# Kernel tuning notes

Hardware: AMD Instinct MI355X
Metric: run time of the kernel (lower is better)

The kernel has to match this reference:

```python
import jax, jax.numpy as jnp
import numpy as np

EPS = 1e-6
NEG_SLOPE = 0.2
LN_EPS = 1e-6


def _evn_nonlinearity(x, wa, ba, wb, bb):
    # x: (..., F, D); norm over the vector axis F (axis=-2)
    norm = jnp.linalg.norm(x, axis=-2, keepdims=True)  # (..., 1, D)
    zero_norm = norm <= EPS
    norm = norm + EPS
    h = jax.nn.leaky_relu(norm @ wa + ba, NEG_SLOPE)   # (..., 1, D//2)
    g = h @ wb + bb                                    # (..., 1, D)
    # skip_connection == 0: rescale direction by learned norm gate
    return jnp.where(zero_norm, x, x / norm * g)


def _layernorm(x, scale, bias):
    mean = jnp.mean(x, axis=-1, keepdims=True)
    var = jnp.var(x, axis=-1, keepdims=True)
    return (x - mean) * jax.lax.rsqrt(var + LN_EPS) * scale + bias


def setup_inputs() -> dict:
    key = jax.random.key(0)
    ks = jax.random.split(key, 12)
    B, N, F, D = 8, 2048, 3, 256
    QK, V, H, Q = 512, 512, 8, 64
    dh, dv = QK // H, V // H
    s = lambda *sh: 1.0 / np.sqrt(sh[0])
    return {
        "x": jax.random.normal(ks[0], (B, N, F, D), jnp.float32),
        "lq": jax.random.normal(ks[1], (Q, QK), jnp.float32) * s(QK),
        "w_kv": jax.random.normal(ks[2], (D, QK), jnp.float32) * s(D),
        "w_evn1a": jax.random.normal(ks[3], (QK, QK // 2), jnp.float32) * s(QK),
        "b_evn1a": jnp.zeros((QK // 2,), jnp.float32),
        "w_evn1b": jax.random.normal(ks[4], (QK // 2, QK), jnp.float32) * s(QK // 2),
        "b_evn1b": jnp.zeros((QK,), jnp.float32),
        "wq": jax.random.normal(ks[5], (QK, H, dh), jnp.float32) * s(QK),
        "wk": jax.random.normal(ks[6], (QK, H, dh), jnp.float32) * s(QK),
        "wv": jax.random.normal(ks[7], (QK, H, dv), jnp.float32) * s(QK),
        "ln_q_scale": jnp.ones((dh,), jnp.float32),
        "ln_q_bias": jnp.zeros((dh,), jnp.float32),
        "ln_k_scale": jnp.ones((dh,), jnp.float32),
        "ln_k_bias": jnp.zeros((dh,), jnp.float32),
        "w_out": jax.random.normal(ks[8], (V, V), jnp.float32) * s(V),
        "w_evn2a": jax.random.normal(ks[9], (V, V // 2), jnp.float32) * s(V),
        "b_evn2a": jnp.zeros((V // 2,), jnp.float32),
        "w_evn2b": jax.random.normal(ks[10], (V // 2, V), jnp.float32) * s(V // 2),
        "b_evn2b": jnp.zeros((V,), jnp.float32),
    }


def reference(x, lq, w_kv, w_evn1a, b_evn1a, w_evn1b, b_evn1b, wq, wk, wv,
              ln_q_scale, ln_q_bias, ln_k_scale, ln_k_bias,
              w_out, w_evn2a, b_evn2a, w_evn2b, b_evn2b):
    B, N, F, _ = x.shape
    H = wq.shape[1]
    # EVLinearLeakyReLU: Dense (no bias) + EVN nonlinearity
    kv = _evn_nonlinearity(x @ w_kv, w_evn1a, b_evn1a, w_evn1b, b_evn1b)  # (B,N,F,QK)
    # invariant features: contract vector axis with its channel-mean
    kv_inv = jnp.einsum('bnfd,bnf->bnd', kv, jnp.mean(kv, axis=-1))       # (B,N,QK)
    q = jnp.einsum('qd,dhe->hqe', lq, wq)          # (H,Q,dh)
    k = jnp.einsum('bnd,dhe->hbne', kv_inv, wk)    # (H,B,N,dh)
    v = jnp.einsum('bnfd,dhe->hbnfe', kv, wv)      # (H,B,N,F,dv)
    # normalize_qk
    q = _layernorm(q, ln_q_scale, ln_q_bias)
    k = _layernorm(k, ln_k_scale, ln_k_bias)
    scale = np.sqrt(k.shape[-1]).astype(np.float32)
    attn = jnp.einsum('hqi,hbki->hbqk', q, k)      # (H,B,Q,N)
    attn = jax.nn.softmax(attn / scale, axis=-1)
    resi = jnp.einsum('hbqk,hbkfd->hbqfd', attn, v)  # (H,B,Q,F,dv)
    # 'h b q f d -> b q f (h d)'
    resi = jnp.moveaxis(resi, 0, -2)
    resi = resi.reshape(*resi.shape[:-2], -1)        # (B,Q,F,V)
    resi = _evn_nonlinearity(resi @ w_out, w_evn2a, b_evn2a, w_evn2b, b_evn2b)
    return resi
```

## Files before the change

### kernel.cpp

```cpp
#include <hip/hip_runtime.h>
#include <hip/hip_bf16.h>

typedef _Float16 f16;
typedef __attribute__((ext_vector_type(8))) _Float16 f16x8;
typedef __attribute__((ext_vector_type(4))) _Float16 f16x4;
typedef __attribute__((ext_vector_type(2))) _Float16 f16x2;
typedef __attribute__((ext_vector_type(4))) float floatx4;

constexpr int B  = 8;
constexpr int N  = 2048;
constexpr int Fv = 3;
constexpr int Dd = 256;
constexpr int QK = 512;
constexpr int Vd = 512;
constexpr int Hh = 8;
constexpr int Qq = 64;
constexpr int DH = 64;
constexpr int NT = B * N;
constexpr float EPS = 1e-6f;
constexpr float NEG = 0.2f;
constexpr float LNE = 1e-6f;

#define DEV static __device__ __forceinline__
DEV void split(float v, f16& h, f16& l) { h = (f16)v; l = (f16)(v - (float)h); }

template<int ASRC, int EPI>
__global__ __launch_bounds__(256) void k_gemm3(
    const float* __restrict__ A32,
    const f16* __restrict__ Ah, const f16* __restrict__ Al,
    const f16* __restrict__ Bh, const f16* __restrict__ Bl,
    int Ndim, int Kdim, void* __restrict__ C1, void* __restrict__ C2,
    const float* __restrict__ e0, const float* __restrict__ e1)
{
    __shared__ __align__(16) f16 Ash[128][72];
    __shared__ __align__(16) f16 Asl[128][72];
    __shared__ __align__(16) f16 Bsh[64][72];
    __shared__ __align__(16) f16 Bsl[64][72];

    const int t = threadIdx.x;
    long row0; int col0, boff;
    if (EPI == 5) { row0 = (long)blockIdx.y * 1536 + (long)blockIdx.x * 128; col0 = 0; boff = blockIdx.y * 64; }
    else          { row0 = (long)blockIdx.x * 128; col0 = blockIdx.y * 64; boff = 0; }

    floatx4 acc0[4], acc1[4];
    #pragma unroll
    for (int nt = 0; nt < 4; ++nt)
        #pragma unroll
        for (int j = 0; j < 4; ++j) { acc0[nt][j] = 0.f; acc1[nt][j] = 0.f; }

    const int L = t & 63, w = t >> 6;
    const int kq = (L >> 4) << 3;

    for (int k0 = 0; k0 < Kdim; k0 += 64) {
        if constexpr (ASRC == 1) {
            #pragma unroll
            for (int j = 0; j < 8; ++j) {
                const int i = t + j * 256;
                const int r = i >> 4, c4 = (i & 15) << 2;
                const floatx4 v = *(const floatx4*)&A32[(row0 + r) * Kdim + k0 + c4];
                f16x4 h4, l4;
                #pragma unroll
                for (int m = 0; m < 4; ++m) { h4[m] = (f16)v[m]; l4[m] = (f16)(v[m] - (float)h4[m]); }
                *(f16x4*)&Ash[r][c4] = h4;
                *(f16x4*)&Asl[r][c4] = l4;
            }
        } else {
            #pragma unroll
            for (int j = 0; j < 4; ++j) {
                const int i = t + j * 256;
                const int r = i >> 3, c8 = (i & 7) << 3;
                *(f16x8*)&Ash[r][c8] = *(const f16x8*)&Ah[(row0 + r) * (long)Kdim + k0 + c8];
                *(f16x8*)&Asl[r][c8] = *(const f16x8*)&Al[(row0 + r) * (long)Kdim + k0 + c8];
            }
        }
        #pragma unroll
        for (int j = 0; j < 2; ++j) {
            const int i = t + j * 256;
            const int r = i >> 3, c8 = (i & 7) << 3;
            *(f16x8*)&Bsh[r][c8] = *(const f16x8*)&Bh[(long)(boff + col0 + r) * Kdim + k0 + c8];
            *(f16x8*)&Bsl[r][c8] = *(const f16x8*)&Bl[(long)(boff + col0 + r) * Kdim + k0 + c8];
        }
        __syncthreads();
        #pragma unroll
        for (int kk = 0; kk < 64; kk += 32) {
            const f16x8 ah0 = *(const f16x8*)&Ash[w * 32 + (L & 15)][kk + kq];
            const f16x8 al0 = *(const f16x8*)&Asl[w * 32 + (L & 15)][kk + kq];
            const f16x8 ah1 = *(const f16x8*)&Ash[w * 32 + 16 + (L & 15)][kk + kq];
            const f16x8 al1 = *(const f16x8*)&Asl[w * 32 + 16 + (L & 15)][kk + kq];
            #pragma unroll
            for (int nt = 0; nt < 4; ++nt) {
                const f16x8 bh = *(const f16x8*)&Bsh[nt * 16 + (L & 15)][kk + kq];
                const f16x8 bl = *(const f16x8*)&Bsl[nt * 16 + (L & 15)][kk + kq];
                acc0[nt] = __builtin_amdgcn_mfma_f32_16x16x32_f16(ah0, bh, acc0[nt], 0, 0, 0);
                acc0[nt] = __builtin_amdgcn_mfma_f32_16x16x32_f16(ah0, bl, acc0[nt], 0, 0, 0);
                acc0[nt] = __builtin_amdgcn_mfma_f32_16x16x32_f16(al0, bh, acc0[nt], 0, 0, 0);
                acc1[nt] = __builtin_amdgcn_mfma_f32_16x16x32_f16(ah1, bh, acc1[nt], 0, 0, 0);
                acc1[nt] = __builtin_amdgcn_mfma_f32_16x16x32_f16(ah1, bl, acc1[nt], 0, 0, 0);
                acc1[nt] = __builtin_amdgcn_mfma_f32_16x16x32_f16(al1, bh, acc1[nt], 0, 0, 0);
            }
        }
        __syncthreads();
    }

    const int cb = L & 15;
    #pragma unroll
    for (int rt = 0; rt < 2; ++rt) {
        const floatx4* acc = rt ? acc1 : acc0;
        const int rb = w * 32 + rt * 16 + ((L >> 4) << 2);
        if constexpr (EPI == 0) {
            f16* Ch = (f16*)C1; f16* Cl = (f16*)C2;
            #pragma unroll
            for (int nt = 0; nt < 4; ++nt)
                #pragma unroll
                for (int r = 0; r < 4; ++r) {
                    f16 h, l; split(acc[nt][r], h, l);
                    const long o = (row0 + rb + r) * (long)Ndim + col0 + nt * 16 + cb;
                    Ch[o] = h; Cl[o] = l;
                }
        } else if constexpr (EPI == 1) {
            f16* Ch = (f16*)C1; f16* Cl = (f16*)C2;
            #pragma unroll
            for (int nt = 0; nt < 4; ++nt) {
                const int col = col0 + nt * 16 + cb;
                const float bias = e0[col];
                #pragma unroll
                for (int r = 0; r < 4; ++r) {
                    float v = acc[nt][r] + bias;
                    v = v > 0.f ? v : NEG * v;
                    f16 h, l; split(v, h, l);
                    const long o = (row0 + rb + r) * (long)Ndim + col;
                    Ch[o] = h; Cl[o] = l;
                }
            }
        } else if constexpr (EPI == 2) {
            float* C = (float*)C1;
            #pragma unroll
            for (int nt = 0; nt < 4; ++nt) {
                const int col = col0 + nt * 16 + cb;
                const float bias = e0[col];
                #pragma unroll
                for (int r = 0; r < 4; ++r)
                    C[(row0 + rb + r) * (long)Ndim + col] = acc[nt][r] + bias;
            }
        } else if constexpr (EPI == 3) {
            f16* Ch = (f16*)C1; f16* Cl = (f16*)C2;
            const int h = blockIdx.y;
            #pragma unroll
            for (int r = 0; r < 4; ++r) {
                float s = 0.f, q = 0.f;
                #pragma unroll
                for (int nt = 0; nt < 4; ++nt) { const float v = acc[nt][r]; s += v; q += v * v; }
                s += __shfl_xor(s, 1); q += __shfl_xor(q, 1);
                s += __shfl_xor(s, 2); q += __shfl_xor(q, 2);
                s += __shfl_xor(s, 4); q += __shfl_xor(q, 4);
                s += __shfl_xor(s, 8); q += __shfl_xor(q, 8);
                const float mean = s * (1.f / 64.f);
                const float var  = q * (1.f / 64.f) - mean * mean;
                const float rs   = rsqrtf(var + LNE);
                #pragma unroll
                for (int nt = 0; nt < 4; ++nt) {
                    const int col = nt * 16 + cb;
                    const float v = (acc[nt][r] - mean) * rs * e0[col] + e1[col];
                    f16 hh, ll; split(v, hh, ll);
                    const long o = ((long)h * NT + row0 + rb + r) * 64 + col;
                    Ch[o] = hh; Cl[o] = ll;
                }
            }
        } else {
            float* C = (float*)C1;
            #pragma unroll
            for (int nt = 0; nt < 4; ++nt)
                #pragma unroll
                for (int r = 0; r < 4; ++r) {
                    const long rr = row0 + rb + r - (long)blockIdx.y * 1536;
                    C[rr * 512 + boff + nt * 16 + cb] = acc[nt][r];
                }
        }
    }
}

__global__ __launch_bounds__(256) void k_attn_mfma(
    const f16* __restrict__ qh, const f16* __restrict__ ql,
    const f16* __restrict__ kh, const f16* __restrict__ kl,
    f16* __restrict__ ath, f16* __restrict__ atl, float* __restrict__ lsum)
{
    __shared__ __align__(16) f16 Qh[64][72], Ql[64][72];
    __shared__ __align__(16) f16 Kh[64][72], Kl[64][72];

    const int t = threadIdx.x;
    const int hb = blockIdx.x;
    const int h = hb >> 3;
    const int L = t & 63, w = t >> 6;
    const int kq = (L >> 4) << 3;

    #pragma unroll
    for (int j = 0; j < 2; ++j) {
        const int i = t + j * 256;
        const int r = i >> 3, c8 = (i & 7) << 3;
        *(f16x8*)&Qh[r][c8] = *(const f16x8*)&qh[((long)h * 64 + r) * 64 + c8];
        *(f16x8*)&Ql[r][c8] = *(const f16x8*)&ql[((long)h * 64 + r) * 64 + c8];
    }
    __syncthreads();

    f16x8 qah[2], qal[2];
    #pragma unroll
    for (int kc = 0; kc < 2; ++kc) {
        qah[kc] = *(const f16x8*)&Qh[w * 16 + (L & 15)][kc * 32 + kq];
        qal[kc] = *(const f16x8*)&Ql[w * 16 + (L & 15)][kc * 32 + kq];
    }

    float psum[4] = {0.f, 0.f, 0.f, 0.f};
    const int rowb = w * 16 + ((L >> 4) << 2);

    for (int n0 = 0; n0 < N; n0 += 64) {
        __syncthreads();
        #pragma unroll
        for (int j = 0; j < 2; ++j) {
            const int i = t + j * 256;
            const int r = i >> 3, c8 = (i & 7) << 3;
            *(f16x8*)&Kh[r][c8] = *(const f16x8*)&kh[((long)hb * N + n0 + r) * 64 + c8];
            *(f16x8*)&Kl[r][c8] = *(const f16x8*)&kl[((long)hb * N + n0 + r) * 64 + c8];
        }
        __syncthreads();

        floatx4 acc[4];
        #pragma unroll
        for (int nt = 0; nt < 4; ++nt)
            #pragma unroll
            for (int j = 0; j < 4; ++j) acc[nt][j] = 0.f;

        #pragma unroll
        for (int kc = 0; kc < 2; ++kc) {
            #pragma unroll
            for (int nt = 0; nt < 4; ++nt) {
                const f16x8 bh = *(const f16x8*)&Kh[nt * 16 + (L & 15)][kc * 32 + kq];
                const f16x8 bl = *(const f16x8*)&Kl[nt * 16 + (L & 15)][kc * 32 + kq];
                acc[nt] = __builtin_amdgcn_mfma_f32_16x16x32_f16(qah[kc], bh, acc[nt], 0, 0, 0);
                acc[nt] = __builtin_amdgcn_mfma_f32_16x16x32_f16(qah[kc], bl, acc[nt], 0, 0, 0);
                acc[nt] = __builtin_amdgcn_mfma_f32_16x16x32_f16(qal[kc], bh, acc[nt], 0, 0, 0);
            }
        }

        #pragma unroll
        for (int nt = 0; nt < 4; ++nt)
            #pragma unroll
            for (int r = 0; r < 4; ++r) {
                const float p = __expf(acc[nt][r] * 0.125f);
                psum[r] += p;
                f16 hh, ll; split(p, hh, ll);
                const long o = ((long)hb * 64 + rowb + r) * N + n0 + nt * 16 + (L & 15);
                ath[o] = hh; atl[o] = ll;
            }
    }

    #pragma unroll
    for (int r = 0; r < 4; ++r) {
        float s = psum[r];
        s += __shfl_xor(s, 1);
        s += __shfl_xor(s, 2);
        s += __shfl_xor(s, 4);
        s += __shfl_xor(s, 8);
        if ((L & 15) == 0) lsum[hb * 64 + rowb + r] = s;
    }
}

__global__ __launch_bounds__(256, 2) void k_gemm3T(
    const f16* __restrict__ Ah, const f16* __restrict__ Al,
    const f16* __restrict__ Bh, const f16* __restrict__ Bl,
    const float* __restrict__ lsum,
    f16* __restrict__ Uh, f16* __restrict__ Ul)
{
    __shared__ __align__(16) f16 Ash[64][72];
    __shared__ __align__(16) f16 Asl[64][72];
    __shared__ __align__(16) f16 Bsh[192][72];
    __shared__ __align__(16) f16 Bsl[192][72];

    const int t = threadIdx.x;
    const int by = blockIdx.x;
    const int hb = by & 63, ct = by >> 6;
    const int b = hb & 7;
    const f16* Abh = Ah + (long)hb * 64 * 2048;
    const f16* Abl = Al + (long)hb * 64 * 2048;
    const f16* Bbh = Bh + (long)b * 2048 * 1536 + ct * 192;
    const f16* Bbl = Bl + (long)b * 2048 * 1536 + ct * 192;

    floatx4 acc[2][6];
    #pragma unroll
    for (int i = 0; i < 2; ++i)
        #pragma unroll
        for (int nt = 0; nt < 6; ++nt)
            #pragma unroll
            for (int j = 0; j < 4; ++j) acc[i][nt][j] = 0.f;

    const int L = t & 63, w = t >> 6;
    const int wr = (w >> 1) << 5;
    const int wc = (w & 1) * 96;
    const int kq = (L >> 4) << 3;
    const int ar = t >> 3, ac = (t & 7) << 3;
    const int k2 = t & 31, c8 = (t >> 5) << 3;

    f16x8 pA0, pA1, pA2, pA3;
    f16x8 pBh0[3], pBh1[3], pBl0[3], pBl1[3];
    {
        pA0 = *(const f16x8*)&Abh[(long)ar * 2048 + ac];
        pA1 = *(const f16x8*)&Abh[(long)(ar + 32) * 2048 + ac];
        pA2 = *(const f16x8*)&Abl[(long)ar * 2048 + ac];
        pA3 = *(const f16x8*)&Abl[(long)(ar + 32) * 2048 + ac];
        #pragma unroll
        for (int g = 0; g < 3; ++g) {
            pBh0[g] = *(const f16x8*)&Bbh[(long)(2 * k2) * 1536 + g * 64 + c8];
            pBh1[g] = *(const f16x8*)&Bbh[(long)(2 * k2 + 1) * 1536 + g * 64 + c8];
            pBl0[g] = *(const f16x8*)&Bbl[(long)(2 * k2) * 1536 + g * 64 + c8];
            pBl1[g] = *(const f16x8*)&Bbl[(long)(2 * k2 + 1) * 1536 + g * 64 + c8];
        }
    }

    for (int k0 = 0; k0 < 2048; k0 += 64) {
        *(f16x8*)&Ash[ar][ac]      = pA0;
        *(f16x8*)&Ash[ar + 32][ac] = pA1;
        *(f16x8*)&Asl[ar][ac]      = pA2;
        *(f16x8*)&Asl[ar + 32][ac] = pA3;
        #pragma unroll
        for (int g = 0; g < 3; ++g)
            #pragma unroll
            for (int j = 0; j < 8; ++j) {
                f16x2 ph; ph[0] = pBh0[g][j]; ph[1] = pBh1[g][j];
                f16x2 pl; pl[0] = pBl0[g][j]; pl[1] = pBl1[g][j];
                *(f16x2*)&Bsh[g * 64 + c8 + j][2 * k2] = ph;
                *(f16x2*)&Bsl[g * 64 + c8 + j][2 * k2] = pl;
            }
        __syncthreads();

        if (k0 + 64 < 2048) {
            const int kn = k0 + 64;
            pA0 = *(const f16x8*)&Abh[(long)ar * 2048 + kn + ac];
            pA1 = *(const f16x8*)&Abh[(long)(ar + 32) * 2048 + kn + ac];
            pA2 = *(const f16x8*)&Abl[(long)ar * 2048 + kn + ac];
            pA3 = *(const f16x8*)&Abl[(long)(ar + 32) * 2048 + kn + ac];
            #pragma unroll
            for (int g = 0; g < 3; ++g) {
                pBh0[g] = *(const f16x8*)&Bbh[(long)(kn + 2 * k2) * 1536 + g * 64 + c8];
                pBh1[g] = *(const f16x8*)&Bbh[(long)(kn + 2 * k2 + 1) * 1536 + g * 64 + c8];
                pBl0[g] = *(const f16x8*)&Bbl[(long)(kn + 2 * k2) * 1536 + g * 64 + c8];
                pBl1[g] = *(const f16x8*)&Bbl[(long)(kn + 2 * k2 + 1) * 1536 + g * 64 + c8];
            }
        }

        #pragma unroll
        for (int kk = 0; kk < 64; kk += 32) {
            const f16x8 ah0 = *(const f16x8*)&Ash[wr + (L & 15)][kk + kq];
            const f16x8 al0 = *(const f16x8*)&Asl[wr + (L & 15)][kk + kq];
            const f16x8 ah1 = *(const f16x8*)&Ash[wr + 16 + (L & 15)][kk + kq];
            const f16x8 al1 = *(const f16x8*)&Asl[wr + 16 + (L & 15)][kk + kq];
            #pragma unroll
            for (int nt = 0; nt < 6; ++nt) {
                const f16x8 bh = *(const f16x8*)&Bsh[wc + nt * 16 + (L & 15)][kk + kq];
                const f16x8 bl = *(const f16x8*)&Bsl[wc + nt * 16 + (L & 15)][kk + kq];
                acc[0][nt] = __builtin_amdgcn_mfma_f32_16x16x32_f16(ah0, bh, acc[0][nt], 0, 0, 0);
                acc[0][nt] = __builtin_amdgcn_mfma_f32_16x16x32_f16(ah0, bl, acc[0][nt], 0, 0, 0);
                acc[0][nt] = __builtin_amdgcn_mfma_f32_16x16x32_f16(al0, bh, acc[0][nt], 0, 0, 0);
                acc[1][nt] = __builtin_amdgcn_mfma_f32_16x16x32_f16(ah1, bh, acc[1][nt], 0, 0, 0);
                acc[1][nt] = __builtin_amdgcn_mfma_f32_16x16x32_f16(ah1, bl, acc[1][nt], 0, 0, 0);
                acc[1][nt] = __builtin_amdgcn_mfma_f32_16x16x32_f16(al1, bh, acc[1][nt], 0, 0, 0);
            }
        }
        __syncthreads();
    }

    const int cb = L & 15;
    #pragma unroll
    for (int rt = 0; rt < 2; ++rt) {
        const int rb = wr + rt * 16 + ((L >> 4) << 2);
        #pragma unroll
        for (int r = 0; r < 4; ++r) {
            const float inv = 1.f / lsum[hb * 64 + rb + r];
            #pragma unroll
            for (int nt = 0; nt < 6; ++nt) {
                f16 h, l; split(acc[rt][nt][r] * inv, h, l);
                const long o = ((long)hb * 64 + rb + r) * 1536 + ct * 192 + wc + nt * 16 + cb;
                Uh[o] = h; Ul[o] = l;
            }
        }
    }
}

__global__ void k_castTpair(const float* __restrict__ s, f16* __restrict__ dh,
                            f16* __restrict__ dl, int K, int Nn)
{
    const long i = (long)blockIdx.x * 256 + threadIdx.x;
    if (i >= (long)K * Nn) return;
    const int k = (int)(i / Nn), n = (int)(i - (long)k * Nn);
    f16 h, l; split(s[i], h, l);
    dh[(long)n * K + k] = h;
    dl[(long)n * K + k] = l;
}

__global__ void k_norm(const f16* __restrict__ kh, const f16* __restrict__ kl,
                       f16* __restrict__ nh, f16* __restrict__ nl)
{
    const long i = (long)blockIdx.x * 256 + threadIdx.x;
    const int tk = (int)(i >> 9), c = (int)(i & 511);
    const long base = (long)tk * 1536 + c;
    const float a = (float)kh[base]        + (float)kl[base];
    const float b = (float)kh[base + 512]  + (float)kl[base + 512];
    const float cc = (float)kh[base + 1024] + (float)kl[base + 1024];
    f16 h, l; split(sqrtf(a * a + b * b + cc * cc) + EPS, h, l);
    nh[i] = h; nl[i] = l;
}

__global__ __launch_bounds__(256) void k_gate(
    f16* __restrict__ kh, f16* __restrict__ kl, const float* __restrict__ g,
    f16* __restrict__ kih, f16* __restrict__ kil)
{
    __shared__ float red[3][4];
    const int t = threadIdx.x;
    const int tk = blockIdx.x;
    float kv[2][3];
    float ps0 = 0.f, ps1 = 0.f, ps2 = 0.f;
    #pragma unroll
    for (int j = 0; j < 2; ++j) {
        const int c = t + j * 256;
        const long base = (long)tk * 1536 + c;
        const float k0 = (float)kh[base]        + (float)kl[base];
        const float k1 = (float)kh[base + 512]  + (float)kl[base + 512];
        const float k2 = (float)kh[base + 1024] + (float)kl[base + 1024];
        const float nr = sqrtf(k0 * k0 + k1 * k1 + k2 * k2);
        const float gv = g[(long)tk * 512 + c];
        const float s = (nr <= EPS) ? 1.f : gv / (nr + EPS);
        kv[j][0] = k0 * s; kv[j][1] = k1 * s; kv[j][2] = k2 * s;
        f16 h, l;
        split(kv[j][0], h, l); kh[base] = h;        kl[base] = l;
        split(kv[j][1], h, l); kh[base + 512] = h;  kl[base + 512] = l;
        split(kv[j][2], h, l); kh[base + 1024] = h; kl[base + 1024] = l;
        ps0 += kv[j][0]; ps1 += kv[j][1]; ps2 += kv[j][2];
    }
    for (int off = 32; off; off >>= 1) {
        ps0 += __shfl_down(ps0, off);
        ps1 += __shfl_down(ps1, off);
        ps2 += __shfl_down(ps2, off);
    }
    if ((t & 63) == 0) { red[0][t >> 6] = ps0; red[1][t >> 6] = ps1; red[2][t >> 6] = ps2; }
    __syncthreads();
    const float m0 = (red[0][0] + red[0][1] + red[0][2] + red[0][3]) * (1.f / 512.f);
    const float m1 = (red[1][0] + red[1][1] + red[1][2] + red[1][3]) * (1.f / 512.f);
    const float m2 = (red[2][0] + red[2][1] + red[2][2] + red[2][3]) * (1.f / 512.f);
    #pragma unroll
    for (int j = 0; j < 2; ++j) {
        const int c = t + j * 256;
        f16 h, l; split(kv[j][0] * m0 + kv[j][1] * m1 + kv[j][2] * m2, h, l);
        kih[(long)tk * 512 + c] = h;
        kil[(long)tk * 512 + c] = l;
    }
}

__global__ __launch_bounds__(256) void k_gate2(
    const f16* __restrict__ rph, const f16* __restrict__ rpl,
    const float* __restrict__ g2, float* __restrict__ out)
{
    const int t = threadIdx.x;
    const int tk = blockIdx.x;
    #pragma unroll
    for (int j = 0; j < 2; ++j) {
        const int c = t + j * 256;
        const long base = (long)tk * 1536 + c;
        const float r0 = (float)rph[base]        + (float)rpl[base];
        const float r1 = (float)rph[base + 512]  + (float)rpl[base + 512];
        const float r2 = (float)rph[base + 1024] + (float)rpl[base + 1024];
        const float nr = sqrtf(r0 * r0 + r1 * r1 + r2 * r2);
        const float gv = g2[(long)tk * 512 + c];
        const float s = (nr <= EPS) ? 1.f : gv / (nr + EPS);
        out[base]        = r0 * s;
        out[base + 512]  = r1 * s;
        out[base + 1024] = r2 * s;
    }
}

__global__ __launch_bounds__(256) void k_qproj(
    const float* __restrict__ lq, const float* __restrict__ wq,
    const float* __restrict__ lns, const float* __restrict__ lnb,
    f16* __restrict__ qh, f16* __restrict__ ql)
{
    __shared__ float cs[QK];
    const int t = threadIdx.x;
    const int qi = blockIdx.x;
    const float* cp = lq + (long)qi * QK;
    for (int i = t; i < QK; i += 256) cs[i] = cp[i];
    __syncthreads();

    float a0 = 0, a1 = 0;
    #pragma unroll 4
    for (int d = 0; d < QK; ++d) {
        const float c = cs[d];
        a0 += c * wq[d * QK + t];
        a1 += c * wq[d * QK + t + 256];
    }
    float s0 = a0, q0 = a0 * a0, s1 = a1, q1 = a1 * a1;
    for (int off = 32; off; off >>= 1) {
        s0 += __shfl_down(s0, off); q0 += __shfl_down(q0, off);
        s1 += __shfl_down(s1, off); q1 += __shfl_down(q1, off);
    }
    s0 = __shfl(s0, 0); q0 = __shfl(q0, 0);
    s1 = __shfl(s1, 0); q1 = __shfl(q1, 0);
    const float mean0 = s0 * (1.f / 64.f), var0 = q0 * (1.f / 64.f) - mean0 * mean0;
    const float mean1 = s1 * (1.f / 64.f), var1 = q1 * (1.f / 64.f) - mean1 * mean1;
    const int e = t & 63;
    const float sc = lns[e], bi = lnb[e];
    const float r0 = (a0 - mean0) * rsqrtf(var0 + LNE) * sc + bi;
    const float r1 = (a1 - mean1) * rsqrtf(var1 + LNE) * sc + bi;
    const int h0 = t >> 6, h1 = h0 + 4;
    f16 h, l;
    split(r0, h, l);
    qh[((long)h0 * Qq + qi) * DH + e] = h;
    ql[((long)h0 * Qq + qi) * DH + e] = l;
    split(r1, h, l);
    qh[((long)h1 * Qq + qi) * DH + e] = h;
    ql[((long)h1 * Qq + qi) * DH + e] = l;
}

extern "C" void kernel_launch(void* const* d_in, const int* in_sizes, int n_in,
                              void* d_out, int out_size, void* d_ws, size_t ws_size,
                              hipStream_t stream)
{
    const float* x    = (const float*)d_in[0];
    const float* lq   = (const float*)d_in[1];
    const float* w_kv = (const float*)d_in[2];
    const float* w1a  = (const float*)d_in[3];
    const float* b1a  = (const float*)d_in[4];
    const float* w1b  = (const float*)d_in[5];
    const float* b1b  = (const float*)d_in[6];
    const float* wq   = (const float*)d_in[7];
    const float* wk   = (const float*)d_in[8];
    const float* wv   = (const float*)d_in[9];
    const float* lqs  = (const float*)d_in[10];
    const float* lqb  = (const float*)d_in[11];
    const float* lks  = (const float*)d_in[12];
    const float* lkb  = (const float*)d_in[13];
    const float* wo   = (const float*)d_in[14];
    const float* w2a  = (const float*)d_in[15];
    const float* b2a  = (const float*)d_in[16];
    const float* w2b  = (const float*)d_in[17];
    const float* b2b  = (const float*)d_in[18];

    char* ws = (char*)d_ws;
    f16* wkvTh = (f16*)(ws + 0);
    f16* wkvTl = (f16*)(ws + 262144);
    f16* w1aTh = (f16*)(ws + 524288);
    f16* w1aTl = (f16*)(ws + 786432);
    f16* w1bTh = (f16*)(ws + 1048576);
    f16* w1bTl = (f16*)(ws + 1310720);
    f16* wkTh  = (f16*)(ws + 1572864);
    f16* wkTl  = (f16*)(ws + 2097152);
    f16* wvTh  = (f16*)(ws + 2621440);
    f16* wvTl  = (f16*)(ws + 3145728);
    f16*   qhp   = (f16*)(ws + 3670016);
    f16*   qlp   = (f16*)(ws + 3735552);
    float* lsum  = (float*)(ws + 3801088);
    f16* woTh  = (f16*)(ws + 3817472);
    f16* woTl  = (f16*)(ws + 4341760);
    f16* w2aTh = (f16*)(ws + 4866048);
    f16* w2aTl = (f16*)(ws + 5128192);
    f16* w2bTh = (f16*)(ws + 5390336);
    f16* w2bTl = (f16*)(ws + 5652480);
    f16* nh    = (f16*)(ws + 6946816);
    f16* nl    = (f16*)(ws + 23724032);
    f16* kih   = nh;
    f16* kil   = nl;
    f16* ath   = (f16*)(ws + 6946816);
    f16* atl   = (f16*)(ws + 23724032);
    f16*   rph  = (f16*)(ws + 6946816);
    f16*   rpl  = (f16*)(ws + 8519680);
    f16*   n2h  = (f16*)(ws + 10092544);
    f16*   n2l  = (f16*)(ws + 10616832);
    f16*   h2h  = (f16*)(ws + 11141120);
    f16*   h2l  = (f16*)(ws + 11403264);
    float* g2   = (float*)(ws + 11665408);
    f16* hbh   = (f16*)(ws + 40501248);
    f16* hbl   = (f16*)(ws + 48889856);
    float* resiT = (float*)(ws + 40501248);
    f16* kvh   = (f16*)(ws + 57278464);
    f16* kvl   = (f16*)(ws + 107610112);
    float* g    = (float*)(ws + 157941760);
    f16* khb   = (f16*)(ws + 157941760);
    f16* klb   = (f16*)(ws + 174718976);
    f16* Uh    = (f16*)(ws + 157941760);
    f16* Ul    = (f16*)(ws + 170524672);
    float* out  = (float*)d_out;

    k_castTpair<<<512,  256, 0, stream>>>(w_kv, wkvTh, wkvTl, Dd, QK);
    k_castTpair<<<512,  256, 0, stream>>>(w1a,  w1aTh, w1aTl, QK, 256);
    k_castTpair<<<512,  256, 0, stream>>>(w1b,  w1bTh, w1bTl, 256, QK);
    k_castTpair<<<1024, 256, 0, stream>>>(wk,   wkTh,  wkTl,  QK, QK);
    k_castTpair<<<1024, 256, 0, stream>>>(wv,   wvTh,  wvTl,  QK, QK);
    k_castTpair<<<1024, 256, 0, stream>>>(wo,   woTh,  woTl,  Vd, Vd);
    k_castTpair<<<512,  256, 0, stream>>>(w2a,  w2aTh, w2aTl, Vd, 256);
    k_castTpair<<<512,  256, 0, stream>>>(w2b,  w2bTh, w2bTl, 256, Vd);

    k_gemm3<1, 0><<<dim3(384, 8), 256, 0, stream>>>(
        x, nullptr, nullptr, wkvTh, wkvTl, QK, Dd, kvh, kvl, nullptr, nullptr);
    k_norm<<<32768, 256, 0, stream>>>(kvh, kvl, nh, nl);
    k_gemm3<0, 1><<<dim3(128, 4), 256, 0, stream>>>(
        nullptr, nh, nl, w1aTh, w1aTl, 256, QK, hbh, hbl, b1a, nullptr);
    k_gemm3<0, 2><<<dim3(128, 8), 256, 0, stream>>>(
        nullptr, hbh, hbl, w1bTh, w1bTl, QK, 256, g, nullptr, b1b, nullptr);
    k_gate<<<NT, 256, 0, stream>>>(kvh, kvl, g, kih, kil);
    k_gemm3<0, 3><<<dim3(128, 8), 256, 0, stream>>>(
        nullptr, kih, kil, wkTh, wkTl, QK, QK, khb, klb, lks, lkb);
    k_qproj<<<Qq, 256, 0, stream>>>(lq, wq, lqs, lqb, qhp, qlp);
    k_attn_mfma<<<Hh * B, 256, 0, stream>>>(qhp, qlp, khb, klb, ath, atl, lsum);
    k_gemm3T<<<64 * 8, 256, 0, stream>>>(ath, atl, kvh, kvl, lsum, Uh, Ul);
    k_gemm3<0, 5><<<dim3(12, 8), 256, 0, stream>>>(
        nullptr, Uh, Ul, wvTh, wvTl, 64, QK, resiT, nullptr, nullptr, nullptr);
    k_gemm3<1, 0><<<dim3(12, 8), 256, 0, stream>>>(
        resiT, nullptr, nullptr, woTh, woTl, Vd, Vd, rph, rpl, nullptr, nullptr);
    k_norm<<<1024, 256, 0, stream>>>(rph, rpl, n2h, n2l);
    k_gemm3<0, 1><<<dim3(4, 4), 256, 0, stream>>>(
        nullptr, n2h, n2l, w2aTh, w2aTl, 256, Vd, h2h, h2l, b2a, nullptr);
    k_gemm3<0, 2><<<dim3(4, 8), 256, 0, stream>>>(
        nullptr, h2h, h2l, w2bTh, w2bTl, Vd, 256, g2, nullptr, b2b, nullptr);
    k_gate2<<<B * Qq, 256, 0, stream>>>(rph, rpl, g2, out);
}
```

Baseline: 654.5 us.

## Retile attention-times-V GEMM to pair two heads sharing the same batch's kv

Each block of the attn·kv GEMM now handles two heads (hb0, hb1) of the same batch, giving 128 rows by 96 columns with 512 threads, where before it handled one head with 64 rows by 192 columns. Each staged kv tile is therefore reused across two heads' attention rows. This is meant to cut global traffic on the large kv operand and raise occupancy through smaller per-thread accumulators. In exchange the A tile is larger, only 384 of the 512 threads stage B, and each block keeps a single-buffer sync pattern.

```diff
diff --git a/kernel.cpp b/kernel.cpp
--- a/kernel.cpp
+++ b/kernel.cpp
@@ -264,85 +264,90 @@
     }
 }
 
-__global__ __launch_bounds__(256, 2) void k_gemm3T(
+__global__ __launch_bounds__(512, 4) void k_gemm3T(
     const f16* __restrict__ Ah, const f16* __restrict__ Al,
     const f16* __restrict__ Bh, const f16* __restrict__ Bl,
     const float* __restrict__ lsum,
     f16* __restrict__ Uh, f16* __restrict__ Ul)
 {
-    __shared__ __align__(16) f16 Ash[64][72];
-    __shared__ __align__(16) f16 Asl[64][72];
-    __shared__ __align__(16) f16 Bsh[192][72];
-    __shared__ __align__(16) f16 Bsl[192][72];
+    __shared__ __align__(16) f16 Ash[128][72];
+    __shared__ __align__(16) f16 Asl[128][72];
+    __shared__ __align__(16) f16 Bsh[96][72];
+    __shared__ __align__(16) f16 Bsl[96][72];
 
     const int t = threadIdx.x;
     const int by = blockIdx.x;
-    const int hb = by & 63, ct = by >> 6;
-    const int b = hb & 7;
-    const f16* Abh = Ah + (long)hb * 64 * 2048;
-    const f16* Abl = Al + (long)hb * 64 * 2048;
-    const f16* Bbh = Bh + (long)b * 2048 * 1536 + ct * 192;
-    const f16* Bbl = Bl + (long)b * 2048 * 1536 + ct * 192;
-
-    floatx4 acc[2][6];
+    const int b = by & 7;
+    const int rest = by >> 3;
+    const int ct = rest & 15;
+    const int hp = rest >> 4;
+    const int hb0 = b + 16 * hp;
+    const int hb1 = hb0 + 8;
+    const f16* A0h = Ah + (long)hb0 * 64 * 2048;
+    const f16* A0l = Al + (long)hb0 * 64 * 2048;
+    const f16* A1h = Ah + (long)hb1 * 64 * 2048;
+    const f16* A1l = Al + (long)hb1 * 64 * 2048;
+    const f16* Bbh = Bh + (long)b * 2048 * 1536 + ct * 96;
+    const f16* Bbl = Bl + (long)b * 2048 * 1536 + ct * 96;
+
+    floatx4 acc[2][3];
     #pragma unroll
     for (int i = 0; i < 2; ++i)
         #pragma unroll
-        for (int nt = 0; nt < 6; ++nt)
+        for (int nt = 0; nt < 3; ++nt)
             #pragma unroll
             for (int j = 0; j < 4; ++j) acc[i][nt][j] = 0.f;
 
     const int L = t & 63, w = t >> 6;
     const int wr = (w >> 1) << 5;
-    const int wc = (w & 1) * 96;
+    const int wc = (w & 1) * 48;
     const int kq = (L >> 4) << 3;
     const int ar = t >> 3, ac = (t & 7) << 3;
     const int k2 = t & 31, c8 = (t >> 5) << 3;
-
-    f16x8 pA0, pA1, pA2, pA3;
-    f16x8 pBh0[3], pBh1[3], pBl0[3], pBl1[3];
+    const bool bstage = t < 384;
+
+    f16x8 pA0h, pA1h, pA0l, pA1l;
+    f16x8 pB0h, pB1h, pB0l, pB1l;
     {
-        pA0 = *(const f16x8*)&Abh[(long)ar * 2048 + ac];
-        pA1 = *(const f16x8*)&Abh[(long)(ar + 32) * 2048 + ac];
-        pA2 = *(const f16x8*)&Abl[(long)ar * 2048 + ac];
-        pA3 = *(const f16x8*)&Abl[(long)(ar + 32) * 2048 + ac];
-        #pragma unroll
-        for (int g = 0; g < 3; ++g) {
-            pBh0[g] = *(const f16x8*)&Bbh[(long)(2 * k2) * 1536 + g * 64 + c8];
-            pBh1[g] = *(const f16x8*)&Bbh[(long)(2 * k2 + 1) * 1536 + g * 64 + c8];
-            pBl0[g] = *(const f16x8*)&Bbl[(long)(2 * k2) * 1536 + g * 64 + c8];
-            pBl1[g] = *(const f16x8*)&Bbl[(long)(2 * k2 + 1) * 1536 + g * 64 + c8];
+        pA0h = *(const f16x8*)&A0h[(long)ar * 2048 + ac];
+        pA1h = *(const f16x8*)&A1h[(long)ar * 2048 + ac];
+        pA0l = *(const f16x8*)&A0l[(long)ar * 2048 + ac];
+        pA1l = *(const f16x8*)&A1l[(long)ar * 2048 + ac];
+        if (bstage) {
+            pB0h = *(const f16x8*)&Bbh[(long)(2 * k2) * 1536 + c8];
+            pB1h = *(const f16x8*)&Bbh[(long)(2 * k2 + 1) * 1536 + c8];
+            pB0l = *(const f16x8*)&Bbl[(long)(2 * k2) * 1536 + c8];
+            pB1l = *(const f16x8*)&Bbl[(long)(2 * k2 + 1) * 1536 + c8];
         }
     }
 
     for (int k0 = 0; k0 < 2048; k0 += 64) {
-        *(f16x8*)&Ash[ar][ac]      = pA0;
-        *(f16x8*)&Ash[ar + 32][ac] = pA1;
-        *(f16x8*)&Asl[ar][ac]      = pA2;
-        *(f16x8*)&Asl[ar + 32][ac] = pA3;
-        #pragma unroll
-        for (int g = 0; g < 3; ++g)
+        *(f16x8*)&Ash[ar][ac]      = pA0h;
+        *(f16x8*)&Ash[ar + 64][ac] = pA1h;
+        *(f16x8*)&Asl[ar][ac]      = pA0l;
+        *(f16x8*)&Asl[ar + 64][ac] = pA1l;
+        if (bstage) {
             #pragma unroll
             for (int j = 0; j < 8; ++j) {
-                f16x2 ph; ph[0] = pBh0[g][j]; ph[1] = pBh1[g][j];
-                f16x2 pl; pl[0] = pBl0[g][j]; pl[1] = pBl1[g][j];
-                *(f16x2*)&Bsh[g * 64 + c8 + j][2 * k2] = ph;
-                *(f16x2*)&Bsl[g * 64 + c8 + j][2 * k2] = pl;
-            }
+                f16x2 ph; ph[0] = pB0h[j]; ph[1] = pB1h[j];
+                f16x2 pl; pl[0] = pB0l[j]; pl[1] = pB1l[j];
+                *(f16x2*)&Bsh[c8 + j][2 * k2] = ph;
+                *(f16x2*)&Bsl[c8 + j][2 * k2] = pl;
+            }
+        }
         __syncthreads();
 
         if (k0 + 64 < 2048) {
             const int kn = k0 + 64;
-            pA0 = *(const f16x8*)&Abh[(long)ar * 2048 + kn + ac];
-            pA1 = *(const f16x8*)&Abh[(long)(ar + 32) * 2048 + kn + ac];
-            pA2 = *(const f16x8*)&Abl[(long)ar * 2048 + kn + ac];
-            pA3 = *(const f16x8*)&Abl[(long)(ar + 32) * 2048 + kn + ac];
-            #pragma unroll
-            for (int g = 0; g < 3; ++g) {
-                pBh0[g] = *(const f16x8*)&Bbh[(long)(kn + 2 * k2) * 1536 + g * 64 + c8];
-                pBh1[g] = *(const f16x8*)&Bbh[(long)(kn + 2 * k2 + 1) * 1536 + g * 64 + c8];
-                pBl0[g] = *(const f16x8*)&Bbl[(long)(kn + 2 * k2) * 1536 + g * 64 + c8];
-                pBl1[g] = *(const f16x8*)&Bbl[(long)(kn + 2 * k2 + 1) * 1536 + g * 64 + c8];
+            pA0h = *(const f16x8*)&A0h[(long)ar * 2048 + kn + ac];
+            pA1h = *(const f16x8*)&A1h[(long)ar * 2048 + kn + ac];
+            pA0l = *(const f16x8*)&A0l[(long)ar * 2048 + kn + ac];
+            pA1l = *(const f16x8*)&A1l[(long)ar * 2048 + kn + ac];
+            if (bstage) {
+                pB0h = *(const f16x8*)&Bbh[(long)(kn + 2 * k2) * 1536 + c8];
+                pB1h = *(const f16x8*)&Bbh[(long)(kn + 2 * k2 + 1) * 1536 + c8];
+                pB0l = *(const f16x8*)&Bbl[(long)(kn + 2 * k2) * 1536 + c8];
+                pB1l = *(const f16x8*)&Bbl[(long)(kn + 2 * k2 + 1) * 1536 + c8];
             }
         }
 
@@ -353,7 +358,7 @@
             const f16x8 ah1 = *(const f16x8*)&Ash[wr + 16 + (L & 15)][kk + kq];
             const f16x8 al1 = *(const f16x8*)&Asl[wr + 16 + (L & 15)][kk + kq];
             #pragma unroll
-            for (int nt = 0; nt < 6; ++nt) {
+            for (int nt = 0; nt < 3; ++nt) {
                 const f16x8 bh = *(const f16x8*)&Bsh[wc + nt * 16 + (L & 15)][kk + kq];
                 const f16x8 bl = *(const f16x8*)&Bsl[wc + nt * 16 + (L & 15)][kk + kq];
                 acc[0][nt] = __builtin_amdgcn_mfma_f32_16x16x32_f16(ah0, bh, acc[0][nt], 0, 0, 0);
@@ -370,14 +375,16 @@
     const int cb = L & 15;
     #pragma unroll
     for (int rt = 0; rt < 2; ++rt) {
-        const int rb = wr + rt * 16 + ((L >> 4) << 2);
+        const int rloc = wr + rt * 16 + ((L >> 4) << 2);
+        const int hb = (rloc < 64) ? hb0 : hb1;
         #pragma unroll
         for (int r = 0; r < 4; ++r) {
-            const float inv = 1.f / lsum[hb * 64 + rb + r];
-            #pragma unroll
-            for (int nt = 0; nt < 6; ++nt) {
+            const int q = (rloc + r) & 63;
+            const float inv = 1.f / lsum[hb * 64 + q];
+            #pragma unroll
+            for (int nt = 0; nt < 3; ++nt) {
                 f16 h, l; split(acc[rt][nt][r] * inv, h, l);
-                const long o = ((long)hb * 64 + rb + r) * 1536 + ct * 192 + wc + nt * 16 + cb;
+                const long o = ((long)hb * 64 + q) * 1536 + ct * 96 + wc + nt * 16 + cb;
                 Uh[o] = h; Ul[o] = l;
             }
         }
@@ -607,7 +614,7 @@
         nullptr, kih, kil, wkTh, wkTl, QK, QK, khb, klb, lks, lkb);
     k_qproj<<<Qq, 256, 0, stream>>>(lq, wq, lqs, lqb, qhp, qlp);
     k_attn_mfma<<<Hh * B, 256, 0, stream>>>(qhp, qlp, khb, klb, ath, atl, lsum);
-    k_gemm3T<<<64 * 8, 256, 0, stream>>>(ath, atl, kvh, kvl, lsum, Uh, Ul);
+    k_gemm3T<<<512, 512, 0, stream>>>(ath, atl, kvh, kvl, lsum, Uh, Ul);
     k_gemm3<0, 5><<<dim3(12, 8), 256, 0, stream>>>(
         nullptr, Uh, Ul, wvTh, wvTl, 64, QK, resiT, nullptr, nullptr, nullptr);
     k_gemm3<1, 0><<<dim3(12, 8), 256, 0, stream>>>(
```

New measurement: 623.8 us. 4.7% less time.
